# Optimization experiments

Measured on AMD Instinct MI355X. Metric: run time of the kernel, lower is better.

The kernel has to match this reference:

```python
import jax, jax.numpy as jnp
import numpy as np

TOP_K = 3
EPS = 1e-12  # F.normalize eps


def _lstm(x, W_ih, W_hh, b_ih, b_hh):
    # x: [B, S, I]; PyTorch gate order i, f, g, o; returns h sequence [B, S, H]
    B = x.shape[0]
    H = W_hh.shape[1]
    xs = jnp.swapaxes(x, 0, 1)  # [S, B, I]
    x_proj = xs @ W_ih.T + b_ih + b_hh  # [S, B, 4H]

    def step(carry, xp):
        h, c = carry
        gates = xp + h @ W_hh.T
        i, f, g, o = jnp.split(gates, 4, axis=-1)
        i = jax.nn.sigmoid(i); f = jax.nn.sigmoid(f)
        g = jnp.tanh(g); o = jax.nn.sigmoid(o)
        c = f * c + i * g
        h = o * jnp.tanh(c)
        return (h, c), h

    init = (jnp.zeros((B, H), x.dtype), jnp.zeros((B, H), x.dtype))
    _, hs = jax.lax.scan(step, init, x_proj)
    return jnp.swapaxes(hs, 0, 1)  # [B, S, H]


def setup_inputs() -> dict:
    key = jax.random.key(0)
    ks = jax.random.split(key, 16)
    B, S, I, H, M, N, O = 4, 256, 512, 1024, 256, 65536, 512
    sc = 0.02
    return {
        "x": jax.random.normal(ks[0], (B, S, I), jnp.float32),
        "keys": jax.random.normal(ks[1], (N, M), jnp.float32),
        "values": jax.random.normal(ks[2], (N, M), jnp.float32),
        "importance": jnp.ones((N,), jnp.float32),
        "W_ih": jax.random.normal(ks[3], (4 * H, I), jnp.float32) * sc,
        "W_hh": jax.random.normal(ks[4], (4 * H, H), jnp.float32) * sc,
        "b_ih": jnp.zeros((4 * H,), jnp.float32),
        "b_hh": jnp.zeros((4 * H,), jnp.float32),
        "Wq": jax.random.normal(ks[5], (M, H), jnp.float32) * sc,
        "bq": jnp.zeros((M,), jnp.float32),
        "Wa": jax.random.normal(ks[6], (1, M), jnp.float32) * sc,
        "ba": jnp.zeros((1,), jnp.float32),
        "Wc": jax.random.normal(ks[7], (M, M), jnp.float32) * sc,
        "bc": jnp.zeros((M,), jnp.float32),
        "Wo": jax.random.normal(ks[8], (O, H + M), jnp.float32) * sc,
        "bo": jnp.zeros((O,), jnp.float32),
    }


def reference(x, keys, values, importance, W_ih, W_hh, b_ih, b_hh,
              Wq, bq, Wa, ba, Wc, bc, Wo, bo):
    # Controller LSTM over the whole sequence
    h = _lstm(x, W_ih, W_hh, b_ih, b_hh)  # [B, S, H]

    # Query projection and cosine similarity against the memory keys
    q = h @ Wq.T + bq  # [B, S, M]
    qn = q / jnp.maximum(jnp.linalg.norm(q, axis=-1, keepdims=True), EPS)
    kn = keys / jnp.maximum(jnp.linalg.norm(keys, axis=-1, keepdims=True), EPS)
    sim = jnp.einsum("bsm,nm->bsn", qn, kn) * importance  # [B, S, N]

    # Top-k retrieval and value gather
    _, top_idx = jax.lax.top_k(sim, TOP_K)  # [B, S, k]
    retrieved = values[top_idx]  # [B, S, k, M]

    # Learned attention over retrieved memories
    att_logits = (retrieved @ Wa.T + ba)[..., 0]  # [B, S, k]
    att = jax.nn.softmax(att_logits, axis=-1)
    mem = jnp.einsum("bsk,bskm->bsm", att, retrieved)
    mem = mem @ Wc.T + bc  # combine_layer

    out = jnp.concatenate([h, mem], axis=-1) @ Wo.T + bo  # [B, S, O]
    return out
```

## Files before the change

### kernel.cpp

```cpp
#include <hip/hip_runtime.h>
#include <hip/hip_bf16.h>
#include <cstdint>
#include <cstddef>

#define BB 4
#define SS 256
#define ID 512
#define HD 1024
#define MD 256
#define NKEY 65536
#define OD 512
#define ROWS 1024
#define NWG_LSTM 256
#define NTH_LSTM 256
#define KPB 2048
#define KSPLITS (NKEY / KPB)

typedef __attribute__((ext_vector_type(8))) short bf16x8;
typedef __attribute__((ext_vector_type(4))) float f32x4;
typedef __attribute__((ext_vector_type(8))) unsigned short u16x8;

__global__ __launch_bounds__(256) void sgemm_nt(
    const float* __restrict__ A, int lda,
    const float* __restrict__ Bm, int ldb,
    float* __restrict__ C, int ldc, int K,
    const float* __restrict__ bias, const float* __restrict__ bias2,
    int accum)
{
    __shared__ float As[64][17];
    __shared__ float Bs[64][17];
    const int t = threadIdx.x;
    const int tx = t & 15, ty = t >> 4;
    const int bm = blockIdx.y << 6, bn = blockIdx.x << 6;
    const int lrow = t >> 2, lk4 = (t & 3) << 2;
    float acc[4][4] = {};

    for (int kb = 0; kb < K; kb += 16) {
        const float4 av = *(const float4*)&A[(size_t)(bm + lrow) * lda + kb + lk4];
        const float4 bv = *(const float4*)&Bm[(size_t)(bn + lrow) * ldb + kb + lk4];
        __syncthreads();
        As[lrow][lk4 + 0] = av.x; As[lrow][lk4 + 1] = av.y;
        As[lrow][lk4 + 2] = av.z; As[lrow][lk4 + 3] = av.w;
        Bs[lrow][lk4 + 0] = bv.x; Bs[lrow][lk4 + 1] = bv.y;
        Bs[lrow][lk4 + 2] = bv.z; Bs[lrow][lk4 + 3] = bv.w;
        __syncthreads();
#pragma unroll
        for (int k = 0; k < 16; ++k) {
            const float a0 = As[4 * ty + 0][k], a1 = As[4 * ty + 1][k];
            const float a2 = As[4 * ty + 2][k], a3 = As[4 * ty + 3][k];
            const float b0 = Bs[4 * tx + 0][k], b1 = Bs[4 * tx + 1][k];
            const float b2 = Bs[4 * tx + 2][k], b3 = Bs[4 * tx + 3][k];
            acc[0][0] += a0 * b0; acc[0][1] += a0 * b1; acc[0][2] += a0 * b2; acc[0][3] += a0 * b3;
            acc[1][0] += a1 * b0; acc[1][1] += a1 * b1; acc[1][2] += a1 * b2; acc[1][3] += a1 * b3;
            acc[2][0] += a2 * b0; acc[2][1] += a2 * b1; acc[2][2] += a2 * b2; acc[2][3] += a2 * b3;
            acc[3][0] += a3 * b0; acc[3][1] += a3 * b1; acc[3][2] += a3 * b2; acc[3][3] += a3 * b3;
        }
    }

#pragma unroll
    for (int i = 0; i < 4; ++i) {
        const int row = bm + 4 * ty + i;
        const int col = bn + 4 * tx;
        float4* cp = (float4*)&C[(size_t)row * ldc + col];
        float4 r;
        if (accum) {
            const float4 old = *cp;
            r.x = old.x + acc[i][0]; r.y = old.y + acc[i][1];
            r.z = old.z + acc[i][2]; r.w = old.w + acc[i][3];
        } else {
            float bx = bias[col + 0], by = bias[col + 1], bz = bias[col + 2], bw = bias[col + 3];
            if (bias2) { bx += bias2[col + 0]; by += bias2[col + 1]; bz += bias2[col + 2]; bw += bias2[col + 3]; }
            r.x = acc[i][0] + bx; r.y = acc[i][1] + by;
            r.z = acc[i][2] + bz; r.w = acc[i][3] + bw;
        }
        *cp = r;
    }
}

__global__ void rownorm(const float* __restrict__ X, const float* __restrict__ imp,
                        float* __restrict__ scale_out, float* __restrict__ Xn, int nrows)
{
    const int row = blockIdx.x * 4 + (threadIdx.x >> 6);
    const int lane = threadIdx.x & 63;
    if (row >= nrows) return;
    float4 v = *(const float4*)&X[(size_t)row * 256 + (lane << 2)];
    float ss = v.x * v.x + v.y * v.y + v.z * v.z + v.w * v.w;
#pragma unroll
    for (int o = 1; o < 64; o <<= 1) ss += __shfl_xor(ss, o);
    float sc = 1.f / fmaxf(sqrtf(ss), 1e-12f);
    if (imp) sc *= imp[row];
    if (scale_out && lane == 0) scale_out[row] = sc;
    if (Xn) {
        v.x *= sc; v.y *= sc; v.z *= sc; v.w *= sc;
        *(float4*)&Xn[(size_t)row * 256 + (lane << 2)] = v;
    }
}

__device__ inline float sigm_f(float x) { return 1.f / (1.f + __expf(-x)); }
__device__ inline float tanh_f(float x) { return 1.f - 2.f / (__expf(2.f * x) + 1.f); }

#define SUBSTEP(B, U, UN, C4, XPC) do {                                           \
    asm volatile("s_waitcnt vmcnt(3)" ::: "memory");                              \
    __builtin_amdgcn_sched_barrier(0);                                            \
    const unsigned* pb_ = rec + (slot << 12) + (B << 10) + (t << 2);              \
    while ((((U.x ^ st) | (U.y ^ st) | (U.z ^ st) | (U.w ^ st)) & 0xFFu) != 0u) { \
        __builtin_amdgcn_s_sleep(1);                                              \
        asm volatile("global_load_dwordx4 %0, %1, off sc0 sc1\n\ts_waitcnt vmcnt(0)" \
                     : "=&v"(U) : "v"(pb_) : "memory");                           \
    }                                                                             \
    {                                                                             \
        float4 hw_;                                                               \
        hw_.x = __uint_as_float(U.x & 0xFFFFFF00u);                               \
        hw_.y = __uint_as_float(U.y & 0xFFFFFF00u);                               \
        hw_.z = __uint_as_float(U.z & 0xFFFFFF00u);                               \
        hw_.w = __uint_as_float(U.w & 0xFFFFFF00u);                               \
        *(float4*)&h_lds[B][t << 2] = hw_;                                        \
    }                                                                             \
    asm volatile("s_waitcnt lgkmcnt(0)" ::: "memory");                            \
    __builtin_amdgcn_sched_barrier(0);                                            \
    __builtin_amdgcn_s_barrier();                                                 \
    {                                                                             \
        const unsigned* pn_ = rec + (((B == 3) ? (slot ^ 1) : slot) << 12)        \
                              + (((B + 1) & 3) << 10) + (t << 2);                 \
        asm volatile("global_load_dwordx4 %0, %1, off sc0 sc1"                    \
                     : "=&v"(UN) : "v"(pn_) : "memory");                          \
    }                                                                             \
    const float* hb_ = &h_lds[B][0];                                              \
    float ax_ = 0.f, ay_ = 0.f, az_ = 0.f, aw_ = 0.f;                             \
    _Pragma("unroll")                                                             \
    for (int j = 0; j < 16; ++j) {                                                \
        const float4 hv_ = *(const float4*)&hb_[(ksub << 2) + (j << 6)];          \
        ax_ += w4[j].x * hv_.x; ay_ += w4[j].y * hv_.y;                           \
        az_ += w4[j].z * hv_.z; aw_ += w4[j].w * hv_.w;                           \
    }                                                                             \
    float sm_ = (ax_ + ay_) + (az_ + aw_);                                        \
    sm_ += __shfl_xor(sm_, 1); sm_ += __shfl_xor(sm_, 2);                         \
    sm_ += __shfl_xor(sm_, 4); sm_ += __shfl_xor(sm_, 8);                         \
    sm_ += XPC;                                                                   \
    const float vi_ = __shfl(sm_, ksub);                                          \
    const float vf_ = __shfl(sm_, ksub + 16);                                     \
    const float vg_ = __shfl(sm_, ksub + 32);                                     \
    const float vo_ = __shfl(sm_, ksub + 48);                                     \
    const float iv_ = sigm_f(vi_), fv_ = sigm_f(vf_);                             \
    const float gv_ = tanh_f(vg_), ov_ = sigm_f(vo_);                             \
    C4 = fv_ * C4 + iv_ * gv_;                                                    \
    const float hvv_ = ov_ * tanh_f(C4);                                          \
    if (lane == 0) {                                                              \
        unsigned* dst_ = rec + ((slot ^ 1) << 12) + (B << 10) + unit;             \
        const unsigned uv_ = (__float_as_uint(hvv_) & 0xFFFFFF00u) |              \
                             ((unsigned)(s + 1) & 0xFFu);                         \
        float* ha_ = &h_all[(size_t)((B << 8) + s) * 1024 + unit];                \
        asm volatile("global_store_dword %0, %1, off sc0 sc1"                     \
                     :: "v"(dst_), "v"(uv_) : "memory");                          \
        asm volatile("global_store_dword %0, %1, off"                             \
                     :: "v"(ha_), "v"(hvv_) : "memory");                          \
    }                                                                             \
    {                                                                             \
        const float* px_ = &xp[(size_t)((B << 8) + sn) * 4096 + wrow];            \
        asm volatile("global_load_dword %0, %1, off"                              \
                     : "=&v"(XPC) : "v"(px_) : "memory");                         \
    }                                                                             \
} while (0)

__global__ __launch_bounds__(256) void lstm_kernel(
    const float* __restrict__ xp, const float* __restrict__ W_hh,
    unsigned* __restrict__ rec, float* __restrict__ h_all)
{
    __shared__ float h_lds[4][1024];
    const int t = threadIdx.x;
    const int wave = t >> 6, lane = t & 63;
    const int gt = lane >> 4, ksub = lane & 15;
    const int unit = (blockIdx.x << 2) + wave;
    const int wrow = (gt << 10) + unit;

    float4 w4[16];
#pragma unroll
    for (int j = 0; j < 16; ++j)
        w4[j] = *(const float4*)&W_hh[(size_t)wrow * 1024 + (ksub << 2) + (j << 6)];

    float c40 = 0.f, c41 = 0.f, c42 = 0.f, c43 = 0.f;
    float xpc0 = xp[(size_t)(0 * 256 + 0) * 4096 + wrow];
    float xpc1 = xp[(size_t)(1 * 256 + 0) * 4096 + wrow];
    float xpc2 = xp[(size_t)(2 * 256 + 0) * 4096 + wrow];
    float xpc3 = xp[(size_t)(3 * 256 + 0) * 4096 + wrow];

    uint4 u0 = make_uint4(~0u, ~0u, ~0u, ~0u);
    uint4 u1 = u0, u2 = u0, u3 = u0;

    {
        const unsigned* p00 = rec + (t << 2);
        asm volatile("global_load_dwordx4 %0, %1, off sc0 sc1\n\ts_waitcnt vmcnt(0)"
                     : "=&v"(u0) : "v"(p00) : "memory");
        __builtin_amdgcn_sched_barrier(0);
    }

    for (int s = 0; s < 256; ++s) {
        const int slot = s & 1;
        const unsigned st = (unsigned)s & 0xFFu;
        const int sn = (s < 255) ? s + 1 : 255;
        SUBSTEP(0, u0, u1, c40, xpc0);
        SUBSTEP(1, u1, u2, c41, xpc1);
        SUBSTEP(2, u2, u3, c42, xpc2);
        SUBSTEP(3, u3, u0, c43, xpc3);
    }
}

#define SWAP1(A, B, IA, IB) { float _t = A; A = B; B = _t; int _u = IA; IA = IB; IB = _u; }
#define INS8G(P, V, ID) do {                                          \
    const float _v = (V); const int _id = (ID);                       \
    if (_v > P##v7) {                                                 \
        P##v7 = _v; P##i7 = _id;                                      \
        if (P##v7 > P##v6) SWAP1(P##v6, P##v7, P##i6, P##i7);         \
        if (P##v6 > P##v5) SWAP1(P##v5, P##v6, P##i5, P##i6);         \
        if (P##v5 > P##v4) SWAP1(P##v4, P##v5, P##i4, P##i5);         \
        if (P##v4 > P##v3) SWAP1(P##v3, P##v4, P##i3, P##i4);         \
        if (P##v3 > P##v2) SWAP1(P##v2, P##v3, P##i2, P##i3);         \
        if (P##v2 > P##v1) SWAP1(P##v1, P##v2, P##i1, P##i2);         \
        if (P##v1 > P##v0) SWAP1(P##v0, P##v1, P##i0, P##i1);         \
    }                                                                 \
} while (0)
#define DECL8(P) float P##v0=-3e38f,P##v1=-3e38f,P##v2=-3e38f,P##v3=-3e38f, \
                       P##v4=-3e38f,P##v5=-3e38f,P##v6=-3e38f,P##v7=-3e38f; \
                 int P##i0=0x7fffffff,P##i1=0x7fffffff,P##i2=0x7fffffff,P##i3=0x7fffffff, \
                     P##i4=0x7fffffff,P##i5=0x7fffffff,P##i6=0x7fffffff,P##i7=0x7fffffff;

__device__ inline unsigned pack_bf16(float a, float b) {
    return (__float_as_uint(a) >> 16) | (__float_as_uint(b) & 0xFFFF0000u);
}

__global__ __launch_bounds__(256) void sim_mfma(
    const float* __restrict__ qn, const float* __restrict__ keys,
    const float* __restrict__ rnk, float* __restrict__ part_v8, int* __restrict__ part_i8)
{
    __shared__ unsigned short k_lds[64 * 264];
    __shared__ float cand_v[256 * 8];
    __shared__ int   cand_i[256 * 8];
    const int t = threadIdx.x;
    const int wave = t >> 6, lane = t & 63;
    const int ks = blockIdx.x, qs = blockIdx.y;
    const int key_base = ks * KPB;
    const int q0 = qs << 6;
    const int qrow = q0 + (wave << 4) + (lane & 15);
    const int kg = lane >> 4;

    bf16x8 bq[8];
#pragma unroll
    for (int kc = 0; kc < 8; ++kc) {
        const float* qp = &qn[(size_t)qrow * 256 + (kc << 5) + (kg << 3)];
        const float4 f0 = *(const float4*)qp;
        const float4 f1 = *(const float4*)(qp + 4);
        union { unsigned int u[4]; bf16x8 h; } cv;
        cv.u[0] = pack_bf16(f0.x, f0.y);
        cv.u[1] = pack_bf16(f0.z, f0.w);
        cv.u[2] = pack_bf16(f1.x, f1.y);
        cv.u[3] = pack_bf16(f1.z, f1.w);
        bq[kc] = cv.h;
    }

    DECL8(t)

    for (int stg = 0; stg < KPB / 64; ++stg) {
        __syncthreads();
#pragma unroll
        for (int i = 0; i < 8; ++i) {
            const int g = (i << 11) + (t << 3);
            const int row = g >> 8, col = g & 255;
            const int krow = key_base + (stg << 6) + row;
            const float sc = rnk[krow];
            const float* kp = &keys[(size_t)krow * 256 + col];
            float4 f0 = *(const float4*)kp;
            float4 f1 = *(const float4*)(kp + 4);
            f0.x *= sc; f0.y *= sc; f0.z *= sc; f0.w *= sc;
            f1.x *= sc; f1.y *= sc; f1.z *= sc; f1.w *= sc;
            union { unsigned int u[4]; u16x8 h; } cv;
            cv.u[0] = pack_bf16(f0.x, f0.y);
            cv.u[1] = pack_bf16(f0.z, f0.w);
            cv.u[2] = pack_bf16(f1.x, f1.y);
            cv.u[3] = pack_bf16(f1.z, f1.w);
            *(u16x8*)&k_lds[row * 264 + col] = cv.h;
        }
        __syncthreads();

#pragma unroll
        for (int kt = 0; kt < 4; ++kt) {
            f32x4 a0 = {0.f, 0.f, 0.f, 0.f};
            f32x4 a1 = {0.f, 0.f, 0.f, 0.f};
#pragma unroll
            for (int kc = 0; kc < 4; ++kc) {
                const bf16x8 af = *(const bf16x8*)&k_lds[((kt << 4) + (lane & 15)) * 264 +
                                                         (kc << 5) + (kg << 3)];
                a0 = __builtin_amdgcn_mfma_f32_16x16x32_bf16(af, bq[kc], a0, 0, 0, 0);
            }
#pragma unroll
            for (int kc = 4; kc < 8; ++kc) {
                const bf16x8 af = *(const bf16x8*)&k_lds[((kt << 4) + (lane & 15)) * 264 +
                                                         (kc << 5) + (kg << 3)];
                a1 = __builtin_amdgcn_mfma_f32_16x16x32_bf16(af, bq[kc], a1, 0, 0, 0);
            }
            const int kidx = key_base + (stg << 6) + (kt << 4) + (kg << 2);
            INS8G(t, a0[0] + a1[0], kidx + 0);
            INS8G(t, a0[1] + a1[1], kidx + 1);
            INS8G(t, a0[2] + a1[2], kidx + 2);
            INS8G(t, a0[3] + a1[3], kidx + 3);
        }
    }

    __syncthreads();
    cand_v[t * 8 + 0] = tv0; cand_i[t * 8 + 0] = ti0;
    cand_v[t * 8 + 1] = tv1; cand_i[t * 8 + 1] = ti1;
    cand_v[t * 8 + 2] = tv2; cand_i[t * 8 + 2] = ti2;
    cand_v[t * 8 + 3] = tv3; cand_i[t * 8 + 3] = ti3;
    cand_v[t * 8 + 4] = tv4; cand_i[t * 8 + 4] = ti4;
    cand_v[t * 8 + 5] = tv5; cand_i[t * 8 + 5] = ti5;
    cand_v[t * 8 + 6] = tv6; cand_i[t * 8 + 6] = ti6;
    cand_v[t * 8 + 7] = tv7; cand_i[t * 8 + 7] = ti7;
    __syncthreads();
    if (t < 64) {
        DECL8(m)
        const int w = t >> 4, c = t & 15;
        for (int g = 0; g < 4; ++g) {
            const int src = ((w << 6) + c + (g << 4)) * 8;
            for (int r = 0; r < 8; ++r)
                INS8G(m, cand_v[src + r], cand_i[src + r]);
        }
        const size_t base = (size_t)(q0 + t) * (KSPLITS * 8) + ks * 8;
        part_v8[base + 0] = mv0; part_i8[base + 0] = mi0;
        part_v8[base + 1] = mv1; part_i8[base + 1] = mi1;
        part_v8[base + 2] = mv2; part_i8[base + 2] = mi2;
        part_v8[base + 3] = mv3; part_i8[base + 3] = mi3;
        part_v8[base + 4] = mv4; part_i8[base + 4] = mi4;
        part_v8[base + 5] = mv5; part_i8[base + 5] = mi5;
        part_v8[base + 6] = mv6; part_i8[base + 6] = mi6;
        part_v8[base + 7] = mv7; part_i8[base + 7] = mi7;
    }
}

__global__ void cand_merge(const float* __restrict__ part_v8, const int* __restrict__ part_i8,
                           int* __restrict__ cand8_i)
{
    const int q = blockIdx.x * 256 + threadIdx.x;
    if (q >= ROWS) return;
    DECL8(c)
    for (int j = 0; j < KSPLITS * 8; ++j)
        INS8G(c, part_v8[(size_t)q * (KSPLITS * 8) + j], part_i8[(size_t)q * (KSPLITS * 8) + j]);
    cand8_i[q * 8 + 0] = ci0; cand8_i[q * 8 + 1] = ci1;
    cand8_i[q * 8 + 2] = ci2; cand8_i[q * 8 + 3] = ci3;
    cand8_i[q * 8 + 4] = ci4; cand8_i[q * 8 + 5] = ci5;
    cand8_i[q * 8 + 6] = ci6; cand8_i[q * 8 + 7] = ci7;
}

__global__ void rescore(const float* __restrict__ qn, const float* __restrict__ keys,
                        const float* __restrict__ rnk, const int* __restrict__ cand8_i,
                        int* __restrict__ top_i)
{
    const int q = blockIdx.x;
    const int lane = threadIdx.x;
    const float4 qv = *(const float4*)&qn[(size_t)q * 256 + (lane << 2)];
    float s0, s1, s2, s3, s4, s5, s6, s7;
    int j0, j1, j2, j3, j4, j5, j6, j7;
#define RES(R, S, J) { J = cand8_i[q * 8 + R]; \
    const float4 kv = *(const float4*)&keys[(size_t)J * 256 + (lane << 2)]; \
    float d = qv.x * kv.x + qv.y * kv.y + qv.z * kv.z + qv.w * kv.w; \
    d += __shfl_xor(d, 1); d += __shfl_xor(d, 2); d += __shfl_xor(d, 4); \
    d += __shfl_xor(d, 8); d += __shfl_xor(d, 16); d += __shfl_xor(d, 32); \
    S = d * rnk[J]; }
    RES(0, s0, j0) RES(1, s1, j1) RES(2, s2, j2) RES(3, s3, j3)
    RES(4, s4, j4) RES(5, s5, j5) RES(6, s6, j6) RES(7, s7, j7)
#undef RES
    if (lane == 0) {
#define BET(SV, JV) if (SV > bv || (SV == bv && JV < bi)) { bv = SV; bi = JV; }
#pragma unroll
        for (int k = 0; k < 3; ++k) {
            float bv = s0; int bi = j0;
            BET(s1, j1) BET(s2, j2) BET(s3, j3) BET(s4, j4)
            BET(s5, j5) BET(s6, j6) BET(s7, j7)
            top_i[q * 3 + k] = bi;
            if (j0 == bi) s0 = -3e38f;
            if (j1 == bi) s1 = -3e38f;
            if (j2 == bi) s2 = -3e38f;
            if (j3 == bi) s3 = -3e38f;
            if (j4 == bi) s4 = -3e38f;
            if (j5 == bi) s5 = -3e38f;
            if (j6 == bi) s6 = -3e38f;
            if (j7 == bi) s7 = -3e38f;
        }
#undef BET
    }
}

__global__ void mem_gather(const int* __restrict__ top_i, const float* __restrict__ values,
                           const float* __restrict__ Wa, const float* __restrict__ ba,
                           float* __restrict__ mem_raw)
{
    const int q = blockIdx.x;
    const int lane = threadIdx.x;
    const float4 wa = *(const float4*)&Wa[lane << 2];
    float4 vr[3];
    float lg[3];
#pragma unroll
    for (int r = 0; r < 3; ++r) {
        const int n = top_i[q * 3 + r];
        const float4 v = *(const float4*)&values[(size_t)n * 256 + (lane << 2)];
        vr[r] = v;
        float d = v.x * wa.x + v.y * wa.y + v.z * wa.z + v.w * wa.w;
#pragma unroll
        for (int o = 1; o < 64; o <<= 1) d += __shfl_xor(d, o);
        lg[r] = d + ba[0];
    }
    const float mx = fmaxf(lg[0], fmaxf(lg[1], lg[2]));
    float e0 = __expf(lg[0] - mx), e1 = __expf(lg[1] - mx), e2 = __expf(lg[2] - mx);
    const float inv = 1.f / (e0 + e1 + e2);
    e0 *= inv; e1 *= inv; e2 *= inv;
    float4 m;
    m.x = e0 * vr[0].x + e1 * vr[1].x + e2 * vr[2].x;
    m.y = e0 * vr[0].y + e1 * vr[1].y + e2 * vr[2].y;
    m.z = e0 * vr[0].z + e1 * vr[1].z + e2 * vr[2].z;
    m.w = e0 * vr[0].w + e1 * vr[1].w + e2 * vr[2].w;
    *(float4*)&mem_raw[(size_t)q * 256 + (lane << 2)] = m;
}

extern "C" void kernel_launch(void* const* d_in, const int* in_sizes, int n_in,
                              void* d_out, int out_size, void* d_ws, size_t ws_size,
                              hipStream_t stream)
{
    (void)in_sizes; (void)n_in; (void)out_size; (void)ws_size;
    const float* x     = (const float*)d_in[0];
    const float* keys  = (const float*)d_in[1];
    const float* values= (const float*)d_in[2];
    const float* imp   = (const float*)d_in[3];
    const float* W_ih  = (const float*)d_in[4];
    const float* W_hh  = (const float*)d_in[5];
    const float* b_ih  = (const float*)d_in[6];
    const float* b_hh  = (const float*)d_in[7];
    const float* Wq    = (const float*)d_in[8];
    const float* bq    = (const float*)d_in[9];
    const float* Wa    = (const float*)d_in[10];
    const float* ba    = (const float*)d_in[11];
    const float* Wc    = (const float*)d_in[12];
    const float* bc    = (const float*)d_in[13];
    const float* Wo    = (const float*)d_in[14];
    const float* bo    = (const float*)d_in[15];
    float* out = (float*)d_out;

    float* ws = (float*)d_ws;
    size_t o = 0;
    float* xp      = ws + o; o += (size_t)1024 * 4096;
    float* h_all   = ws + o; o += (size_t)1024 * 1024;
    unsigned* rec  = (unsigned*)(ws + o); o += 2 * 4096;
    float* rnk     = ws + o; o += NKEY;
    float* qbuf    = ws + o; o += (size_t)ROWS * 256;
    float* qn      = ws + o; o += (size_t)ROWS * 256;
    float* part_v8 = ws + o; o += (size_t)ROWS * KSPLITS * 8;
    int*   part_i8 = (int*)(ws + o); o += (size_t)ROWS * KSPLITS * 8;
    int*   cand8_i = (int*)(ws + o); o += ROWS * 8;
    int*   top_i   = (int*)(ws + o); o += 4096;
    float* mem_raw = ws + o; o += (size_t)ROWS * 256;
    float* memb    = ws + o; o += (size_t)ROWS * 256;

    hipMemsetAsync(rec, 0, 2 * 4096 * 4, stream);

    rownorm<<<NKEY / 4, 256, 0, stream>>>(keys, imp, rnk, nullptr, NKEY);

    sgemm_nt<<<dim3(64, 16), 256, 0, stream>>>(x, ID, W_ih, ID, xp, 4096, ID, b_ih, b_hh, 0);

    lstm_kernel<<<NWG_LSTM, NTH_LSTM, 0, stream>>>(xp, W_hh, rec, h_all);

    sgemm_nt<<<dim3(4, 16), 256, 0, stream>>>(h_all, HD, Wq, HD, qbuf, MD, HD, bq, nullptr, 0);

    rownorm<<<ROWS / 4, 256, 0, stream>>>(qbuf, nullptr, nullptr, qn, ROWS);

    sim_mfma<<<dim3(KSPLITS, 16), 256, 0, stream>>>(qn, keys, rnk, part_v8, part_i8);
    cand_merge<<<ROWS / 256, 256, 0, stream>>>(part_v8, part_i8, cand8_i);
    rescore<<<ROWS, 64, 0, stream>>>(qn, keys, rnk, cand8_i, top_i);

    mem_gather<<<ROWS, 64, 0, stream>>>(top_i, values, Wa, ba, mem_raw);

    sgemm_nt<<<dim3(4, 16), 256, 0, stream>>>(mem_raw, MD, Wc, MD, memb, MD, MD, bc, nullptr, 0);

    sgemm_nt<<<dim3(8, 16), 256, 0, stream>>>(h_all, HD, Wo, HD + MD, out, OD, HD, bo, nullptr, 0);
    sgemm_nt<<<dim3(8, 16), 256, 0, stream>>>(memb, MD, Wo + HD, HD + MD, out, OD, MD, nullptr, nullptr, 1);
}
```

Before: 1.377 ms.

## Pair batch substeps in LSTM recurrence and widen input-projection GEMM tile

The persistent LSTM kernel now handles two batch elements per barrier-synchronised substep instead of one. This halves the number of workgroup barriers and cross-workgroup flag polls per timestep and issues the h-vector loads in pairs. Separately, the input projection uses a dedicated 64x128-tile SGEMM with the dimensions hardcoded. The pairing lengthens the dependency chain inside each substep and raises register pressure, and the new GEMM only works for these fixed shapes.

```diff
diff --git a/kernel.cpp b/kernel.cpp
--- a/kernel.cpp
+++ b/kernel.cpp
@@ -77,6 +77,65 @@
     }
 }
 
+__global__ __launch_bounds__(256) void sgemm_nt_w(
+    const float* __restrict__ A, const float* __restrict__ Bm,
+    float* __restrict__ C, const float* __restrict__ bias, const float* __restrict__ bias2)
+{
+    __shared__ float As[16][64];
+    __shared__ float Bs[16][128];
+    const int t = threadIdx.x;
+    const int tx = t & 15, ty = t >> 4;
+    const int bm = blockIdx.y << 6, bn = blockIdx.x << 7;
+    const int arow = t & 63, akq = t >> 6;
+    const int brow = t & 127, bkq = t >> 7;
+    float acc[4][8] = {};
+
+    for (int kb = 0; kb < 512; kb += 16) {
+        const float4 av  = *(const float4*)&A[(size_t)(bm + arow) * 512 + kb + (akq << 2)];
+        const float4 bv0 = *(const float4*)&Bm[(size_t)(bn + brow) * 512 + kb + (bkq << 3)];
+        const float4 bv1 = *(const float4*)&Bm[(size_t)(bn + brow) * 512 + kb + (bkq << 3) + 4];
+        __syncthreads();
+        As[(akq << 2) + 0][arow] = av.x; As[(akq << 2) + 1][arow] = av.y;
+        As[(akq << 2) + 2][arow] = av.z; As[(akq << 2) + 3][arow] = av.w;
+        Bs[(bkq << 3) + 0][brow] = bv0.x; Bs[(bkq << 3) + 1][brow] = bv0.y;
+        Bs[(bkq << 3) + 2][brow] = bv0.z; Bs[(bkq << 3) + 3][brow] = bv0.w;
+        Bs[(bkq << 3) + 4][brow] = bv1.x; Bs[(bkq << 3) + 5][brow] = bv1.y;
+        Bs[(bkq << 3) + 6][brow] = bv1.z; Bs[(bkq << 3) + 7][brow] = bv1.w;
+        __syncthreads();
+#pragma unroll
+        for (int k = 0; k < 16; ++k) {
+            const float4 a  = *(const float4*)&As[k][ty << 2];
+            const float4 b0 = *(const float4*)&Bs[k][tx << 3];
+            const float4 b1 = *(const float4*)&Bs[k][(tx << 3) + 4];
+            acc[0][0] += a.x * b0.x; acc[0][1] += a.x * b0.y; acc[0][2] += a.x * b0.z; acc[0][3] += a.x * b0.w;
+            acc[0][4] += a.x * b1.x; acc[0][5] += a.x * b1.y; acc[0][6] += a.x * b1.z; acc[0][7] += a.x * b1.w;
+            acc[1][0] += a.y * b0.x; acc[1][1] += a.y * b0.y; acc[1][2] += a.y * b0.z; acc[1][3] += a.y * b0.w;
+            acc[1][4] += a.y * b1.x; acc[1][5] += a.y * b1.y; acc[1][6] += a.y * b1.z; acc[1][7] += a.y * b1.w;
+            acc[2][0] += a.z * b0.x; acc[2][1] += a.z * b0.y; acc[2][2] += a.z * b0.z; acc[2][3] += a.z * b0.w;
+            acc[2][4] += a.z * b1.x; acc[2][5] += a.z * b1.y; acc[2][6] += a.z * b1.z; acc[2][7] += a.z * b1.w;
+            acc[3][0] += a.w * b0.x; acc[3][1] += a.w * b0.y; acc[3][2] += a.w * b0.z; acc[3][3] += a.w * b0.w;
+            acc[3][4] += a.w * b1.x; acc[3][5] += a.w * b1.y; acc[3][6] += a.w * b1.z; acc[3][7] += a.w * b1.w;
+        }
+    }
+
+#pragma unroll
+    for (int i = 0; i < 4; ++i) {
+        const int row = bm + (ty << 2) + i;
+        const int col = bn + (tx << 3);
+        float4 r0, r1;
+        r0.x = acc[i][0] + bias[col + 0] + bias2[col + 0];
+        r0.y = acc[i][1] + bias[col + 1] + bias2[col + 1];
+        r0.z = acc[i][2] + bias[col + 2] + bias2[col + 2];
+        r0.w = acc[i][3] + bias[col + 3] + bias2[col + 3];
+        r1.x = acc[i][4] + bias[col + 4] + bias2[col + 4];
+        r1.y = acc[i][5] + bias[col + 5] + bias2[col + 5];
+        r1.z = acc[i][6] + bias[col + 6] + bias2[col + 6];
+        r1.w = acc[i][7] + bias[col + 7] + bias2[col + 7];
+        *(float4*)&C[(size_t)row * 4096 + col] = r0;
+        *(float4*)&C[(size_t)row * 4096 + col + 4] = r1;
+    }
+}
+
 __global__ void rownorm(const float* __restrict__ X, const float* __restrict__ imp,
                         float* __restrict__ scale_out, float* __restrict__ Xn, int nrows)
 {
@@ -99,33 +158,8 @@
 __device__ inline float sigm_f(float x) { return 1.f / (1.f + __expf(-x)); }
 __device__ inline float tanh_f(float x) { return 1.f - 2.f / (__expf(2.f * x) + 1.f); }
 
-#define SUBSTEP(B, U, UN, C4, XPC) do {                                           \
-    asm volatile("s_waitcnt vmcnt(3)" ::: "memory");                              \
-    __builtin_amdgcn_sched_barrier(0);                                            \
-    const unsigned* pb_ = rec + (slot << 12) + (B << 10) + (t << 2);              \
-    while ((((U.x ^ st) | (U.y ^ st) | (U.z ^ st) | (U.w ^ st)) & 0xFFu) != 0u) { \
-        __builtin_amdgcn_s_sleep(1);                                              \
-        asm volatile("global_load_dwordx4 %0, %1, off sc0 sc1\n\ts_waitcnt vmcnt(0)" \
-                     : "=&v"(U) : "v"(pb_) : "memory");                           \
-    }                                                                             \
-    {                                                                             \
-        float4 hw_;                                                               \
-        hw_.x = __uint_as_float(U.x & 0xFFFFFF00u);                               \
-        hw_.y = __uint_as_float(U.y & 0xFFFFFF00u);                               \
-        hw_.z = __uint_as_float(U.z & 0xFFFFFF00u);                               \
-        hw_.w = __uint_as_float(U.w & 0xFFFFFF00u);                               \
-        *(float4*)&h_lds[B][t << 2] = hw_;                                        \
-    }                                                                             \
-    asm volatile("s_waitcnt lgkmcnt(0)" ::: "memory");                            \
-    __builtin_amdgcn_sched_barrier(0);                                            \
-    __builtin_amdgcn_s_barrier();                                                 \
-    {                                                                             \
-        const unsigned* pn_ = rec + (((B == 3) ? (slot ^ 1) : slot) << 12)        \
-                              + (((B + 1) & 3) << 10) + (t << 2);                 \
-        asm volatile("global_load_dwordx4 %0, %1, off sc0 sc1"                    \
-                     : "=&v"(UN) : "v"(pn_) : "memory");                          \
-    }                                                                             \
-    const float* hb_ = &h_lds[B][0];                                              \
+#define GATECOMP(BIDX, UREG, C4, XPC, HVOUT) do {                                 \
+    const float* hb_ = &h_lds[BIDX][0];                                           \
     float ax_ = 0.f, ay_ = 0.f, az_ = 0.f, aw_ = 0.f;                             \
     _Pragma("unroll")                                                             \
     for (int j = 0; j < 16; ++j) {                                                \
@@ -144,21 +178,74 @@
     const float iv_ = sigm_f(vi_), fv_ = sigm_f(vf_);                             \
     const float gv_ = tanh_f(vg_), ov_ = sigm_f(vo_);                             \
     C4 = fv_ * C4 + iv_ * gv_;                                                    \
-    const float hvv_ = ov_ * tanh_f(C4);                                          \
-    if (lane == 0) {                                                              \
-        unsigned* dst_ = rec + ((slot ^ 1) << 12) + (B << 10) + unit;             \
-        const unsigned uv_ = (__float_as_uint(hvv_) & 0xFFFFFF00u) |              \
-                             ((unsigned)(s + 1) & 0xFFu);                         \
-        float* ha_ = &h_all[(size_t)((B << 8) + s) * 1024 + unit];                \
-        asm volatile("global_store_dword %0, %1, off sc0 sc1"                     \
-                     :: "v"(dst_), "v"(uv_) : "memory");                          \
-        asm volatile("global_store_dword %0, %1, off"                             \
-                     :: "v"(ha_), "v"(hvv_) : "memory");                          \
+    HVOUT = ov_ * tanh_f(C4);                                                     \
+} while (0)
+
+#define SUBSTEP2(B0, B1, NB0, NB1, NSLOT, UA, UB, UNA, UNB, C4A, C4B, XPA, XPB) do { \
+    asm volatile("s_waitcnt vmcnt(6)" ::: "memory");                              \
+    __builtin_amdgcn_sched_barrier(0);                                            \
+    const unsigned* pa_ = rec + (slot << 12) + (B0 << 10) + (t << 2);             \
+    const unsigned* pb_ = rec + (slot << 12) + (B1 << 10) + (t << 2);             \
+    while ((((UA.x ^ st) | (UA.y ^ st) | (UA.z ^ st) | (UA.w ^ st) |              \
+             (UB.x ^ st) | (UB.y ^ st) | (UB.z ^ st) | (UB.w ^ st)) & 0xFFu) != 0u) { \
+        __builtin_amdgcn_s_sleep(1);                                              \
+        asm volatile("global_load_dwordx4 %0, %2, off sc0 sc1\n\t"                \
+                     "global_load_dwordx4 %1, %3, off sc0 sc1\n\t"                \
+                     "s_waitcnt vmcnt(0)"                                         \
+                     : "=&v"(UA), "=&v"(UB) : "v"(pa_), "v"(pb_) : "memory");     \
     }                                                                             \
     {                                                                             \
-        const float* px_ = &xp[(size_t)((B << 8) + sn) * 4096 + wrow];            \
+        float4 ha_w, hb_w;                                                        \
+        ha_w.x = __uint_as_float(UA.x & 0xFFFFFF00u);                             \
+        ha_w.y = __uint_as_float(UA.y & 0xFFFFFF00u);                             \
+        ha_w.z = __uint_as_float(UA.z & 0xFFFFFF00u);                             \
+        ha_w.w = __uint_as_float(UA.w & 0xFFFFFF00u);                             \
+        hb_w.x = __uint_as_float(UB.x & 0xFFFFFF00u);                             \
+        hb_w.y = __uint_as_float(UB.y & 0xFFFFFF00u);                             \
+        hb_w.z = __uint_as_float(UB.z & 0xFFFFFF00u);                             \
+        hb_w.w = __uint_as_float(UB.w & 0xFFFFFF00u);                             \
+        *(float4*)&h_lds[B0][t << 2] = ha_w;                                      \
+        *(float4*)&h_lds[B1][t << 2] = hb_w;                                      \
+    }                                                                             \
+    asm volatile("s_waitcnt lgkmcnt(0)" ::: "memory");                            \
+    __builtin_amdgcn_sched_barrier(0);                                            \
+    __builtin_amdgcn_s_barrier();                                                 \
+    {                                                                             \
+        const unsigned* na_ = rec + ((NSLOT) << 12) + (NB0 << 10) + (t << 2);     \
+        const unsigned* nb_ = rec + ((NSLOT) << 12) + (NB1 << 10) + (t << 2);     \
+        asm volatile("global_load_dwordx4 %0, %1, off sc0 sc1"                    \
+                     : "=&v"(UNA) : "v"(na_) : "memory");                         \
+        asm volatile("global_load_dwordx4 %0, %1, off sc0 sc1"                    \
+                     : "=&v"(UNB) : "v"(nb_) : "memory");                         \
+    }                                                                             \
+    float hva_, hvb_;                                                             \
+    GATECOMP(B0, UA, C4A, XPA, hva_);                                             \
+    GATECOMP(B1, UB, C4B, XPB, hvb_);                                             \
+    if (lane == 0) {                                                              \
+        unsigned* da_ = rec + ((slot ^ 1) << 12) + (B0 << 10) + unit;             \
+        unsigned* db_ = rec + ((slot ^ 1) << 12) + (B1 << 10) + unit;             \
+        const unsigned ua_ = (__float_as_uint(hva_) & 0xFFFFFF00u) |              \
+                             ((unsigned)(s + 1) & 0xFFu);                         \
+        const unsigned ub_ = (__float_as_uint(hvb_) & 0xFFFFFF00u) |              \
+                             ((unsigned)(s + 1) & 0xFFu);                         \
+        float* haa_ = &h_all[(size_t)((B0 << 8) + s) * 1024 + unit];              \
+        float* hab_ = &h_all[(size_t)((B1 << 8) + s) * 1024 + unit];              \
+        asm volatile("global_store_dword %0, %1, off sc0 sc1"                     \
+                     :: "v"(da_), "v"(ua_) : "memory");                           \
+        asm volatile("global_store_dword %0, %1, off"                             \
+                     :: "v"(haa_), "v"(hva_) : "memory");                         \
+        asm volatile("global_store_dword %0, %1, off sc0 sc1"                     \
+                     :: "v"(db_), "v"(ub_) : "memory");                           \
+        asm volatile("global_store_dword %0, %1, off"                             \
+                     :: "v"(hab_), "v"(hvb_) : "memory");                         \
+    }                                                                             \
+    {                                                                             \
+        const float* pxa_ = &xp[(size_t)((B0 << 8) + sn) * 4096 + wrow];          \
+        const float* pxb_ = &xp[(size_t)((B1 << 8) + sn) * 4096 + wrow];          \
         asm volatile("global_load_dword %0, %1, off"                              \
-                     : "=&v"(XPC) : "v"(px_) : "memory");                         \
+                     : "=&v"(XPA) : "v"(pxa_) : "memory");                        \
+        asm volatile("global_load_dword %0, %1, off"                              \
+                     : "=&v"(XPB) : "v"(pxb_) : "memory");                        \
     }                                                                             \
 } while (0)
 
@@ -189,8 +276,12 @@
 
     {
         const unsigned* p00 = rec + (t << 2);
-        asm volatile("global_load_dwordx4 %0, %1, off sc0 sc1\n\ts_waitcnt vmcnt(0)"
-                     : "=&v"(u0) : "v"(p00) : "memory");
+        const unsigned* p01 = rec + (1 << 10) + (t << 2);
+        asm volatile(
+            "global_load_dwordx4 %0, %2, off sc0 sc1\n\t"
+            "global_load_dwordx4 %1, %3, off sc0 sc1\n\t"
+            "s_waitcnt vmcnt(0)"
+            : "=&v"(u0), "=&v"(u1) : "v"(p00), "v"(p01) : "memory");
         __builtin_amdgcn_sched_barrier(0);
     }
 
@@ -198,10 +289,8 @@
         const int slot = s & 1;
         const unsigned st = (unsigned)s & 0xFFu;
         const int sn = (s < 255) ? s + 1 : 255;
-        SUBSTEP(0, u0, u1, c40, xpc0);
-        SUBSTEP(1, u1, u2, c41, xpc1);
-        SUBSTEP(2, u2, u3, c42, xpc2);
-        SUBSTEP(3, u3, u0, c43, xpc3);
+        SUBSTEP2(0, 1, 2, 3, slot,     u0, u1, u2, u3, c40, c41, xpc0, xpc1);
+        SUBSTEP2(2, 3, 0, 1, slot ^ 1, u2, u3, u0, u1, c42, c43, xpc2, xpc3);
     }
 }
 
@@ -461,7 +550,7 @@
 
     rownorm<<<NKEY / 4, 256, 0, stream>>>(keys, imp, rnk, nullptr, NKEY);
 
-    sgemm_nt<<<dim3(64, 16), 256, 0, stream>>>(x, ID, W_ih, ID, xp, 4096, ID, b_ih, b_hh, 0);
+    sgemm_nt_w<<<dim3(32, 16), 256, 0, stream>>>(x, W_ih, xp, b_ih, b_hh);
 
     lstm_kernel<<<NWG_LSTM, NTH_LSTM, 0, stream>>>(xp, W_hh, rec, h_all);
 
```

Result: slower. 1.554 ms (+12.9%).

## Double query rows per sim block and widen input-projection GEMM tile

Applied to the files above, without the earlier changes.

The similarity kernel now handles 128 query rows per workgroup using two MFMA accumulator sets that share each LDS key fragment. This halves the number of times keys are loaded from global memory and converted to bf16, and the candidate buffers now reuse the key LDS region. The key staging loop is rearranged so each thread loads one row segment. A new specialised 64x128-tile SGEMM replaces the generic one for the x·W_ih projection to improve reuse. The cost is higher register pressure from the doubled accumulator, query-fragment and top-8 state, which could lower occupancy.

```diff
diff --git a/kernel.cpp b/kernel.cpp
--- a/kernel.cpp
+++ b/kernel.cpp
@@ -74,6 +74,65 @@
             r.z = acc[i][2] + bz; r.w = acc[i][3] + bw;
         }
         *cp = r;
+    }
+}
+
+__global__ __launch_bounds__(256) void sgemm_nt_w(
+    const float* __restrict__ A, const float* __restrict__ Bm,
+    float* __restrict__ C, const float* __restrict__ bias, const float* __restrict__ bias2)
+{
+    __shared__ float As[16][64];
+    __shared__ float Bs[16][128];
+    const int t = threadIdx.x;
+    const int tx = t & 15, ty = t >> 4;
+    const int bm = blockIdx.y << 6, bn = blockIdx.x << 7;
+    const int arow = t & 63, akq = t >> 6;
+    const int brow = t & 127, bkq = t >> 7;
+    float acc[4][8] = {};
+
+    for (int kb = 0; kb < 512; kb += 16) {
+        const float4 av  = *(const float4*)&A[(size_t)(bm + arow) * 512 + kb + (akq << 2)];
+        const float4 bv0 = *(const float4*)&Bm[(size_t)(bn + brow) * 512 + kb + (bkq << 3)];
+        const float4 bv1 = *(const float4*)&Bm[(size_t)(bn + brow) * 512 + kb + (bkq << 3) + 4];
+        __syncthreads();
+        As[(akq << 2) + 0][arow] = av.x; As[(akq << 2) + 1][arow] = av.y;
+        As[(akq << 2) + 2][arow] = av.z; As[(akq << 2) + 3][arow] = av.w;
+        Bs[(bkq << 3) + 0][brow] = bv0.x; Bs[(bkq << 3) + 1][brow] = bv0.y;
+        Bs[(bkq << 3) + 2][brow] = bv0.z; Bs[(bkq << 3) + 3][brow] = bv0.w;
+        Bs[(bkq << 3) + 4][brow] = bv1.x; Bs[(bkq << 3) + 5][brow] = bv1.y;
+        Bs[(bkq << 3) + 6][brow] = bv1.z; Bs[(bkq << 3) + 7][brow] = bv1.w;
+        __syncthreads();
+#pragma unroll
+        for (int k = 0; k < 16; ++k) {
+            const float4 a  = *(const float4*)&As[k][ty << 2];
+            const float4 b0 = *(const float4*)&Bs[k][tx << 3];
+            const float4 b1 = *(const float4*)&Bs[k][(tx << 3) + 4];
+            acc[0][0] += a.x * b0.x; acc[0][1] += a.x * b0.y; acc[0][2] += a.x * b0.z; acc[0][3] += a.x * b0.w;
+            acc[0][4] += a.x * b1.x; acc[0][5] += a.x * b1.y; acc[0][6] += a.x * b1.z; acc[0][7] += a.x * b1.w;
+            acc[1][0] += a.y * b0.x; acc[1][1] += a.y * b0.y; acc[1][2] += a.y * b0.z; acc[1][3] += a.y * b0.w;
+            acc[1][4] += a.y * b1.x; acc[1][5] += a.y * b1.y; acc[1][6] += a.y * b1.z; acc[1][7] += a.y * b1.w;
+            acc[2][0] += a.z * b0.x; acc[2][1] += a.z * b0.y; acc[2][2] += a.z * b0.z; acc[2][3] += a.z * b0.w;
+            acc[2][4] += a.z * b1.x; acc[2][5] += a.z * b1.y; acc[2][6] += a.z * b1.z; acc[2][7] += a.z * b1.w;
+            acc[3][0] += a.w * b0.x; acc[3][1] += a.w * b0.y; acc[3][2] += a.w * b0.z; acc[3][3] += a.w * b0.w;
+            acc[3][4] += a.w * b1.x; acc[3][5] += a.w * b1.y; acc[3][6] += a.w * b1.z; acc[3][7] += a.w * b1.w;
+        }
+    }
+
+#pragma unroll
+    for (int i = 0; i < 4; ++i) {
+        const int row = bm + (ty << 2) + i;
+        const int col = bn + (tx << 3);
+        float4 r0, r1;
+        r0.x = acc[i][0] + bias[col + 0] + bias2[col + 0];
+        r0.y = acc[i][1] + bias[col + 1] + bias2[col + 1];
+        r0.z = acc[i][2] + bias[col + 2] + bias2[col + 2];
+        r0.w = acc[i][3] + bias[col + 3] + bias2[col + 3];
+        r1.x = acc[i][4] + bias[col + 4] + bias2[col + 4];
+        r1.y = acc[i][5] + bias[col + 5] + bias2[col + 5];
+        r1.z = acc[i][6] + bias[col + 6] + bias2[col + 6];
+        r1.w = acc[i][7] + bias[col + 7] + bias2[col + 7];
+        *(float4*)&C[(size_t)row * 4096 + col] = r0;
+        *(float4*)&C[(size_t)row * 4096 + col + 4] = r1;
     }
 }
 
@@ -233,93 +292,105 @@
     const float* __restrict__ rnk, float* __restrict__ part_v8, int* __restrict__ part_i8)
 {
     __shared__ unsigned short k_lds[64 * 264];
-    __shared__ float cand_v[256 * 8];
-    __shared__ int   cand_i[256 * 8];
     const int t = threadIdx.x;
     const int wave = t >> 6, lane = t & 63;
     const int ks = blockIdx.x, qs = blockIdx.y;
     const int key_base = ks * KPB;
-    const int q0 = qs << 6;
-    const int qrow = q0 + (wave << 4) + (lane & 15);
+    const int q0 = qs << 7;
+    const int qrowA = q0 + (wave << 4) + (lane & 15);
+    const int qrowB = qrowA + 64;
     const int kg = lane >> 4;
 
-    bf16x8 bq[8];
+    bf16x8 bqA[8], bqB[8];
 #pragma unroll
     for (int kc = 0; kc < 8; ++kc) {
-        const float* qp = &qn[(size_t)qrow * 256 + (kc << 5) + (kg << 3)];
-        const float4 f0 = *(const float4*)qp;
-        const float4 f1 = *(const float4*)(qp + 4);
-        union { unsigned int u[4]; bf16x8 h; } cv;
-        cv.u[0] = pack_bf16(f0.x, f0.y);
-        cv.u[1] = pack_bf16(f0.z, f0.w);
-        cv.u[2] = pack_bf16(f1.x, f1.y);
-        cv.u[3] = pack_bf16(f1.z, f1.w);
-        bq[kc] = cv.h;
-    }
-
-    DECL8(t)
+        const float* qpA = &qn[(size_t)qrowA * 256 + (kc << 5) + (kg << 3)];
+        const float* qpB = &qn[(size_t)qrowB * 256 + (kc << 5) + (kg << 3)];
+        const float4 a0 = *(const float4*)qpA;
+        const float4 a1 = *(const float4*)(qpA + 4);
+        const float4 b0 = *(const float4*)qpB;
+        const float4 b1 = *(const float4*)(qpB + 4);
+        union { unsigned int u[4]; bf16x8 h; } ca, cb;
+        ca.u[0] = pack_bf16(a0.x, a0.y); ca.u[1] = pack_bf16(a0.z, a0.w);
+        ca.u[2] = pack_bf16(a1.x, a1.y); ca.u[3] = pack_bf16(a1.z, a1.w);
+        cb.u[0] = pack_bf16(b0.x, b0.y); cb.u[1] = pack_bf16(b0.z, b0.w);
+        cb.u[2] = pack_bf16(b1.x, b1.y); cb.u[3] = pack_bf16(b1.z, b1.w);
+        bqA[kc] = ca.h; bqB[kc] = cb.h;
+    }
+
+    DECL8(tA)
+    DECL8(tB)
+
+    const int srow = t >> 2, scol0 = (t & 3) << 6;
 
     for (int stg = 0; stg < KPB / 64; ++stg) {
         __syncthreads();
-#pragma unroll
-        for (int i = 0; i < 8; ++i) {
-            const int g = (i << 11) + (t << 3);
-            const int row = g >> 8, col = g & 255;
-            const int krow = key_base + (stg << 6) + row;
+        {
+            const int krow = key_base + (stg << 6) + srow;
             const float sc = rnk[krow];
-            const float* kp = &keys[(size_t)krow * 256 + col];
-            float4 f0 = *(const float4*)kp;
-            float4 f1 = *(const float4*)(kp + 4);
-            f0.x *= sc; f0.y *= sc; f0.z *= sc; f0.w *= sc;
-            f1.x *= sc; f1.y *= sc; f1.z *= sc; f1.w *= sc;
-            union { unsigned int u[4]; u16x8 h; } cv;
-            cv.u[0] = pack_bf16(f0.x, f0.y);
-            cv.u[1] = pack_bf16(f0.z, f0.w);
-            cv.u[2] = pack_bf16(f1.x, f1.y);
-            cv.u[3] = pack_bf16(f1.z, f1.w);
-            *(u16x8*)&k_lds[row * 264 + col] = cv.h;
+            const float* kp = &keys[(size_t)krow * 256 + scol0];
+#pragma unroll
+            for (int i = 0; i < 8; ++i) {
+                float4 f0 = *(const float4*)(kp + (i << 3));
+                float4 f1 = *(const float4*)(kp + (i << 3) + 4);
+                f0.x *= sc; f0.y *= sc; f0.z *= sc; f0.w *= sc;
+                f1.x *= sc; f1.y *= sc; f1.z *= sc; f1.w *= sc;
+                union { unsigned int u[4]; u16x8 h; } cv;
+                cv.u[0] = pack_bf16(f0.x, f0.y);
+                cv.u[1] = pack_bf16(f0.z, f0.w);
+                cv.u[2] = pack_bf16(f1.x, f1.y);
+                cv.u[3] = pack_bf16(f1.z, f1.w);
+                *(u16x8*)&k_lds[srow * 264 + scol0 + (i << 3)] = cv.h;
+            }
         }
         __syncthreads();
 
 #pragma unroll
         for (int kt = 0; kt < 4; ++kt) {
-            f32x4 a0 = {0.f, 0.f, 0.f, 0.f};
-            f32x4 a1 = {0.f, 0.f, 0.f, 0.f};
-#pragma unroll
-            for (int kc = 0; kc < 4; ++kc) {
+            f32x4 aA = {0.f, 0.f, 0.f, 0.f};
+            f32x4 aB = {0.f, 0.f, 0.f, 0.f};
+#pragma unroll
+            for (int kc = 0; kc < 8; ++kc) {
                 const bf16x8 af = *(const bf16x8*)&k_lds[((kt << 4) + (lane & 15)) * 264 +
                                                          (kc << 5) + (kg << 3)];
-                a0 = __builtin_amdgcn_mfma_f32_16x16x32_bf16(af, bq[kc], a0, 0, 0, 0);
-            }
-#pragma unroll
-            for (int kc = 4; kc < 8; ++kc) {
-                const bf16x8 af = *(const bf16x8*)&k_lds[((kt << 4) + (lane & 15)) * 264 +
-                                                         (kc << 5) + (kg << 3)];
-                a1 = __builtin_amdgcn_mfma_f32_16x16x32_bf16(af, bq[kc], a1, 0, 0, 0);
+                aA = __builtin_amdgcn_mfma_f32_16x16x32_bf16(af, bqA[kc], aA, 0, 0, 0);
+                aB = __builtin_amdgcn_mfma_f32_16x16x32_bf16(af, bqB[kc], aB, 0, 0, 0);
             }
             const int kidx = key_base + (stg << 6) + (kt << 4) + (kg << 2);
-            INS8G(t, a0[0] + a1[0], kidx + 0);
-            INS8G(t, a0[1] + a1[1], kidx + 1);
-            INS8G(t, a0[2] + a1[2], kidx + 2);
-            INS8G(t, a0[3] + a1[3], kidx + 3);
-        }
-    }
-
+            INS8G(tA, aA[0], kidx + 0); INS8G(tB, aB[0], kidx + 0);
+            INS8G(tA, aA[1], kidx + 1); INS8G(tB, aB[1], kidx + 1);
+            INS8G(tA, aA[2], kidx + 2); INS8G(tB, aB[2], kidx + 2);
+            INS8G(tA, aA[3], kidx + 3); INS8G(tB, aB[3], kidx + 3);
+        }
+    }
+
+    float* cand_v = (float*)k_lds;
+    int*   cand_i = (int*)(k_lds + 8192);
     __syncthreads();
-    cand_v[t * 8 + 0] = tv0; cand_i[t * 8 + 0] = ti0;
-    cand_v[t * 8 + 1] = tv1; cand_i[t * 8 + 1] = ti1;
-    cand_v[t * 8 + 2] = tv2; cand_i[t * 8 + 2] = ti2;
-    cand_v[t * 8 + 3] = tv3; cand_i[t * 8 + 3] = ti3;
-    cand_v[t * 8 + 4] = tv4; cand_i[t * 8 + 4] = ti4;
-    cand_v[t * 8 + 5] = tv5; cand_i[t * 8 + 5] = ti5;
-    cand_v[t * 8 + 6] = tv6; cand_i[t * 8 + 6] = ti6;
-    cand_v[t * 8 + 7] = tv7; cand_i[t * 8 + 7] = ti7;
+    cand_v[t * 8 + 0] = tAv0; cand_i[t * 8 + 0] = tAi0;
+    cand_v[t * 8 + 1] = tAv1; cand_i[t * 8 + 1] = tAi1;
+    cand_v[t * 8 + 2] = tAv2; cand_i[t * 8 + 2] = tAi2;
+    cand_v[t * 8 + 3] = tAv3; cand_i[t * 8 + 3] = tAi3;
+    cand_v[t * 8 + 4] = tAv4; cand_i[t * 8 + 4] = tAi4;
+    cand_v[t * 8 + 5] = tAv5; cand_i[t * 8 + 5] = tAi5;
+    cand_v[t * 8 + 6] = tAv6; cand_i[t * 8 + 6] = tAi6;
+    cand_v[t * 8 + 7] = tAv7; cand_i[t * 8 + 7] = tAi7;
+    cand_v[(256 + t) * 8 + 0] = tBv0; cand_i[(256 + t) * 8 + 0] = tBi0;
+    cand_v[(256 + t) * 8 + 1] = tBv1; cand_i[(256 + t) * 8 + 1] = tBi1;
+    cand_v[(256 + t) * 8 + 2] = tBv2; cand_i[(256 + t) * 8 + 2] = tBi2;
+    cand_v[(256 + t) * 8 + 3] = tBv3; cand_i[(256 + t) * 8 + 3] = tBi3;
+    cand_v[(256 + t) * 8 + 4] = tBv4; cand_i[(256 + t) * 8 + 4] = tBi4;
+    cand_v[(256 + t) * 8 + 5] = tBv5; cand_i[(256 + t) * 8 + 5] = tBi5;
+    cand_v[(256 + t) * 8 + 6] = tBv6; cand_i[(256 + t) * 8 + 6] = tBi6;
+    cand_v[(256 + t) * 8 + 7] = tBv7; cand_i[(256 + t) * 8 + 7] = tBi7;
     __syncthreads();
-    if (t < 64) {
+    if (t < 128) {
         DECL8(m)
-        const int w = t >> 4, c = t & 15;
+        const int tt = t & 63;
+        const int setoff = (t < 64) ? 0 : 256;
+        const int w = tt >> 4, c = tt & 15;
         for (int g = 0; g < 4; ++g) {
-            const int src = ((w << 6) + c + (g << 4)) * 8;
+            const int src = (setoff + (w << 6) + (g << 4) + c) * 8;
             for (int r = 0; r < 8; ++r)
                 INS8G(m, cand_v[src + r], cand_i[src + r]);
         }
@@ -461,7 +532,7 @@
 
     rownorm<<<NKEY / 4, 256, 0, stream>>>(keys, imp, rnk, nullptr, NKEY);
 
-    sgemm_nt<<<dim3(64, 16), 256, 0, stream>>>(x, ID, W_ih, ID, xp, 4096, ID, b_ih, b_hh, 0);
+    sgemm_nt_w<<<dim3(32, 16), 256, 0, stream>>>(x, W_ih, xp, b_ih, b_hh);
 
     lstm_kernel<<<NWG_LSTM, NTH_LSTM, 0, stream>>>(xp, W_hh, rec, h_all);
 
@@ -469,7 +540,7 @@
 
     rownorm<<<ROWS / 4, 256, 0, stream>>>(qbuf, nullptr, nullptr, qn, ROWS);
 
-    sim_mfma<<<dim3(KSPLITS, 16), 256, 0, stream>>>(qn, keys, rnk, part_v8, part_i8);
+    sim_mfma<<<dim3(KSPLITS, 8), 256, 0, stream>>>(qn, keys, rnk, part_v8, part_i8);
     cand_merge<<<ROWS / 256, 256, 0, stream>>>(part_v8, part_i8, cand8_i);
     rescore<<<ROWS, 64, 0, stream>>>(qn, keys, rnk, cand8_i, top_i);
 
```

Measured after the change: 1.491 ms. +8.3%, slower.
